# Performance work log

Hardware: AMD Instinct MI355X
Metric: run time of the kernel (lower is better)

Reference implementation:

```python
import jax, jax.numpy as jnp
import numpy as np

N_E = 4096
E_DIM = 512
LEGACY = 0.2


def setup_inputs() -> dict:
    key = jax.random.key(0)
    k1, k2 = jax.random.split(key)
    B, T = 32, 512
    key_soft = jax.random.normal(k1, (B, T, E_DIM), dtype=jnp.float32)
    zero_ts_mask = jnp.zeros((B,), dtype=bool)
    # embedding table has 1 + n_e rows, uniform(-1/n_e, 1/n_e)
    emb = jax.random.uniform(k2, (N_E + 1, E_DIM), dtype=jnp.float32,
                             minval=-1.0 / N_E, maxval=1.0 / N_E)
    return {"key_soft": key_soft, "emb": emb, "zero_ts_mask": zero_ts_mask}


def _neighbor_scan(d, zero_ts_mask):
    # d: [B, T, N+1] squared distances (no grad needed for indices)
    n_e = d.shape[-1] - 1
    ind0 = jnp.clip(jnp.argmin(d[:, 0, :], axis=1), 0, n_e - 1)
    ind0 = jnp.where(zero_ts_mask, 0, ind0)

    def step(ind, d_t):  # ind: [B], d_t: [B, N+1]
        d_here = jnp.take_along_axis(d_t, ind[:, None], axis=1)[:, 0]
        ind_next = jnp.clip(ind + 1, 0, n_e - 1)
        d_next = jnp.take_along_axis(d_t, ind_next[:, None], axis=1)[:, 0]
        ind_new = jnp.where(d_here <= d_next, ind, ind_next)
        return ind_new, ind_new

    d_rest = jnp.transpose(d[:, 1:, :], (1, 0, 2))  # [T-1, B, N+1]
    _, inds_rest = jax.lax.scan(step, ind0, d_rest)
    # [B, T]
    return jnp.concatenate([ind0[:, None], inds_rest.T], axis=1)


def reference(key_soft, emb, zero_ts_mask):
    B, T, D = key_soft.shape
    n_e = emb.shape[0] - 1
    ks_flat = key_soft.reshape(-1, D)
    # squared euclidean distance to every codebook row: [B*T, n_e+1]
    d = (jnp.sum(ks_flat ** 2, axis=1, keepdims=True)
         + jnp.sum(emb ** 2, axis=1)
         - 2.0 * jnp.einsum('bd,nd->bn', ks_flat, emb))
    d_ng = jax.lax.stop_gradient(d)
    min_indices = jnp.argmin(d_ng, axis=1)  # [B*T]
    encoding_indices = _neighbor_scan(d_ng.reshape(B, T, n_e + 1), zero_ts_mask)
    ind_flat = encoding_indices.reshape(-1)

    key_hard_here = emb[ind_flat].reshape(B, T, D)
    key_hard_next = emb[jnp.clip(ind_flat + 1, 0, n_e - 1)].reshape(B, T, D)
    key_min = emb[min_indices].reshape(B, T, D)

    sg = jax.lax.stop_gradient
    ks_sg = sg(key_soft)
    loss_here_base = (jnp.sum((ks_sg - key_hard_here) ** 2, axis=-1) * LEGACY
                      + jnp.sum((key_soft - sg(key_hard_here)) ** 2, axis=-1))
    loss_next_base = (jnp.sum((ks_sg - key_hard_next) ** 2, axis=-1) * LEGACY
                      + jnp.sum((key_soft - sg(key_hard_next)) ** 2, axis=-1))
    loss_min_indices = (jnp.sum((ks_sg - key_min) ** 2, axis=-1)
                        + jnp.sum((key_soft - sg(key_min)) ** 2, axis=-1) * LEGACY)
    loss_here = loss_here_base - jnp.where(loss_min_indices < loss_here_base,
                                           loss_min_indices, 0.0)
    loss_next = loss_next_base - jnp.where(loss_min_indices < loss_next_base,
                                           loss_min_indices, 0.0)

    # straight-through estimator
    key_hard = key_soft + sg(key_hard_here - key_soft)

    v = jnp.max(jnp.max(encoding_indices, axis=1) - jnp.min(encoding_indices, axis=1))
    return key_hard, encoding_indices, v, loss_here, loss_next
```

## Files before the change

kernel.cpp:

```cpp
#include <hip/hip_runtime.h>
#include <cstdint>
#include <cstddef>

#define N_E    4096
#define NCOL   4097
#define DEMB   512
#define BROWS  16384
#define TLEN   512
#define BB     32
#define NTM    128
#define NTN    33
#define NWG    (NTM*NTN)

typedef __attribute__((ext_vector_type(8))) short short8;
typedef __attribute__((ext_vector_type(4))) float f4;

#define WS_KSQ   0
#define WS_ESQ   (WS_KSQ + BROWS*4)
#define WS_PMVB  (WS_ESQ + 4160*4)
#define WS_PMIB  (WS_PMVB + NTN*BROWS*4)
#define WS_DFB   (WS_PMIB + NTN*BROWS*4)
#define WS_DLB   (WS_DFB + NTN*BROWS*4)
#define WS_PMVF  (WS_DLB + NTN*BROWS*4)
#define WS_PMIF  (WS_PMVF + BROWS*4)
#define WS_ENC   (WS_PMIF + BROWS*4)
#define WS_VMAX  (WS_ENC + BROWS*4)
#define WS_MOVE  (WS_VMAX + 512)

__device__ __forceinline__ void cvtpair(float x0, float x1, unsigned int& h, unsigned int& l) {
    asm("v_cvt_pk_bf16_f32 %0, %1, %2" : "=v"(h) : "v"(x0), "v"(x1));
    float h0 = __uint_as_float(h << 16);
    float h1 = __uint_as_float(h & 0xFFFF0000u);
    float l0 = x0 - h0, l1 = x1 - h1;
    asm("v_cvt_pk_bf16_f32 %0, %1, %2" : "=v"(l) : "v"(l0), "v"(l1));
}

__global__ __launch_bounds__(256) void k_sq(const float* __restrict__ ks,
                                            const float* __restrict__ emb,
                                            float* __restrict__ ksq,
                                            float* __restrict__ esq) {
    const int w = threadIdx.x >> 6, lane = threadIdx.x & 63;
    const int row = blockIdx.x * 4 + w;
    if (row >= BROWS + NCOL) return;
    const float* src = (row < BROWS) ? (ks + (size_t)row * DEMB)
                                     : (emb + (size_t)(row - BROWS) * DEMB);
    float4 v1 = *(const float4*)(src + lane * 8);
    float4 v2 = *(const float4*)(src + lane * 8 + 4);
    float s = v1.x*v1.x + v1.y*v1.y + v1.z*v1.z + v1.w*v1.w
            + v2.x*v2.x + v2.y*v2.y + v2.z*v2.z + v2.w*v2.w;
    #pragma unroll
    for (int off = 32; off; off >>= 1) s += __shfl_down(s, off, 64);
    if (lane == 0) {
        if (row < BROWS) ksq[row] = s;
        else             esq[row - BROWS] = s;
    }
}

__global__ __launch_bounds__(256, 2) void k_dist(const float* __restrict__ ks,
                                                 const float* __restrict__ emb,
                                                 const float* __restrict__ ksq,
                                                 const float* __restrict__ esq,
                                                 float* __restrict__ pminvB,
                                                 int*   __restrict__ pminiB,
                                                 float* __restrict__ dfB,
                                                 float* __restrict__ dlB,
                                                 unsigned short* __restrict__ mb16) {
    const int t   = threadIdx.x;
    const int bid = blockIdx.x;
    const int swz = (bid & 7) * (NWG / 8) + (bid >> 3);
    const int mt  = swz / NTN, nt = swz % NTN;
    const int row0 = mt * 128, n0 = nt * 128;

    __shared__ short lds[2][4][128 * 40];

    const int sr = t >> 1, sh = t & 1;
    const float* ap = ks + (size_t)(row0 + sr) * DEMB + sh * 16;
    const int bc = min(n0 + sr, NCOL - 1);
    const float* bp = emb + (size_t)bc * DEMB + sh * 16;
    const int wA = sr * 40 + sh * 16;

    const int w = t >> 6, lane = t & 63;
    const int wm = w >> 1, wn = w & 1;
    const int lq = lane >> 4, lr = lane & 15;
    int aoff[4], boff[4];
    #pragma unroll
    for (int i = 0; i < 4; ++i) aoff[i] = (wm*64 + i*16 + lr)*40 + lq*8;
    #pragma unroll
    for (int j = 0; j < 4; ++j) boff[j] = (wn*64 + j*16 + lr)*40 + lq*8;

    f4 acc[4][4];
    const f4 fz = {0.f, 0.f, 0.f, 0.f};
    #pragma unroll
    for (int i = 0; i < 4; ++i)
        #pragma unroll
        for (int j = 0; j < 4; ++j) acc[i][j] = fz;

    float4 la0, la1, la2, la3, lb0, lb1, lb2, lb3;

    auto do_loads = [&](int s) {
        const float* p = ap + s * 32;
        la0 = *(const float4*)p;       la1 = *(const float4*)(p + 4);
        la2 = *(const float4*)(p + 8); la3 = *(const float4*)(p + 12);
        const float* q = bp + s * 32;
        lb0 = *(const float4*)q;       lb1 = *(const float4*)(q + 4);
        lb2 = *(const float4*)(q + 8); lb3 = *(const float4*)(q + 12);
    };
    auto do_cw = [&](int cb) {
        unsigned int h0,h1,h2,h3,h4,h5,h6,h7, g0,g1,g2,g3,g4,g5,g6,g7;
        cvtpair(la0.x, la0.y, h0, g0); cvtpair(la0.z, la0.w, h1, g1);
        cvtpair(la1.x, la1.y, h2, g2); cvtpair(la1.z, la1.w, h3, g3);
        cvtpair(la2.x, la2.y, h4, g4); cvtpair(la2.z, la2.w, h5, g5);
        cvtpair(la3.x, la3.y, h6, g6); cvtpair(la3.z, la3.w, h7, g7);
        *(uint4*)(&lds[cb][0][wA])     = (uint4){h0,h1,h2,h3};
        *(uint4*)(&lds[cb][0][wA + 8]) = (uint4){h4,h5,h6,h7};
        *(uint4*)(&lds[cb][1][wA])     = (uint4){g0,g1,g2,g3};
        *(uint4*)(&lds[cb][1][wA + 8]) = (uint4){g4,g5,g6,g7};
        cvtpair(lb0.x, lb0.y, h0, g0); cvtpair(lb0.z, lb0.w, h1, g1);
        cvtpair(lb1.x, lb1.y, h2, g2); cvtpair(lb1.z, lb1.w, h3, g3);
        cvtpair(lb2.x, lb2.y, h4, g4); cvtpair(lb2.z, lb2.w, h5, g5);
        cvtpair(lb3.x, lb3.y, h6, g6); cvtpair(lb3.z, lb3.w, h7, g7);
        *(uint4*)(&lds[cb][2][wA])     = (uint4){h0,h1,h2,h3};
        *(uint4*)(&lds[cb][2][wA + 8]) = (uint4){h4,h5,h6,h7};
        *(uint4*)(&lds[cb][3][wA])     = (uint4){g0,g1,g2,g3};
        *(uint4*)(&lds[cb][3][wA + 8]) = (uint4){g4,g5,g6,g7};
    };
    auto do_mm = [&](int cb) {
        short8 fAh[4], fAl[4], fBh[4], fBl[4];
        #pragma unroll
        for (int i = 0; i < 4; ++i) {
            fAh[i] = *(const short8*)(&lds[cb][0][aoff[i]]);
            fAl[i] = *(const short8*)(&lds[cb][1][aoff[i]]);
        }
        #pragma unroll
        for (int j = 0; j < 4; ++j) {
            fBh[j] = *(const short8*)(&lds[cb][2][boff[j]]);
            fBl[j] = *(const short8*)(&lds[cb][3][boff[j]]);
        }
        #pragma unroll
        for (int i = 0; i < 4; ++i)
            #pragma unroll
            for (int j = 0; j < 4; ++j)
                acc[i][j] = __builtin_amdgcn_mfma_f32_16x16x32_bf16(fAh[i], fBh[j], acc[i][j], 0, 0, 0);
        #pragma unroll
        for (int i = 0; i < 4; ++i)
            #pragma unroll
            for (int j = 0; j < 4; ++j)
                acc[i][j] = __builtin_amdgcn_mfma_f32_16x16x32_bf16(fAh[i], fBl[j], acc[i][j], 0, 0, 0);
        #pragma unroll
        for (int i = 0; i < 4; ++i)
            #pragma unroll
            for (int j = 0; j < 4; ++j)
                acc[i][j] = __builtin_amdgcn_mfma_f32_16x16x32_bf16(fAl[i], fBh[j], acc[i][j], 0, 0, 0);
    };

    do_loads(0); do_cw(0); __syncthreads();
    for (int s2 = 0; s2 < 7; ++s2) {
        do_loads(2*s2 + 1); do_mm(0); do_cw(1); __syncthreads();
        do_loads(2*s2 + 2); do_mm(1); do_cw(0); __syncthreads();
    }
    do_loads(15); do_mm(0); do_cw(1); __syncthreads();
    do_mm(1);
    __syncthreads();

    float* sv0 = (float*)&lds[0][0][0];
    int*   si0 = (int*)(sv0 + 256);
    float* sdl = (float*)(si0 + 256);
    float* sdf = sdl + 128;
    float* sd0 = sdf + 128;
    float* sd1 = sd0 + 128;

    const int colC = n0 + wn * 64;
    float esqv[4];
    #pragma unroll
    for (int j = 0; j < 4; ++j) esqv[j] = esq[min(colC + j*16 + lr, NCOL - 1)];

    #pragma unroll
    for (int i = 0; i < 4; ++i) {
        #pragma unroll
        for (int r2 = 0; r2 < 4; ++r2) {
            const int rowl = wm*64 + i*16 + lq*4 + r2;
            const int R = row0 + rowl;
            const float kq = ksq[R];
            float dj[4];
            #pragma unroll
            for (int j = 0; j < 4; ++j) {
                float dd = fmaf(-2.f, acc[i][j][r2], kq + esqv[j]);
                dj[j] = (colC + j*16 + lr <= NCOL - 1) ? dd : 3.0e38f;
            }
            float bv = dj[0]; int bi = colC + lr;
            #pragma unroll
            for (int j = 1; j < 4; ++j) {
                int c = colC + j*16 + lr;
                if (dj[j] < bv || (dj[j] == bv && c < bi)) { bv = dj[j]; bi = c; }
            }
            #pragma unroll
            for (int off = 1; off < 16; off <<= 1) {
                float ov = __shfl_xor(bv, off, 64); int oi = __shfl_xor(bi, off, 64);
                if (ov < bv || (ov == bv && oi < bi)) { bv = ov; bi = oi; }
            }
            if (lr == 0) {
                sv0[rowl*2 + wn] = bv; si0[rowl*2 + wn] = bi;
                if (wn == 1) sdf[rowl] = dj[0];
                else         sd0[rowl] = dj[0];
            }
            if (lr == 15) {
                if (wn == 0) sdl[rowl] = dj[3];
                else         sd1[rowl] = dj[3];
            }
            #pragma unroll
            for (int j = 0; j < 4; ++j) {
                float left = __shfl_up(dj[j], 1, 64);
                if (j > 0) {
                    float ph = __shfl(dj[j-1], (lane & 48) | 15, 64);
                    if (lr == 0) left = ph;
                }
                bool pred = (lr == 0 && j == 0) ? false : (left > dj[j]);
                unsigned long long bal = __ballot(pred);
                const int Cb = colC + j * 16;
                if (lr == 0 && Cb < 4096)
                    mb16[(size_t)R*256 + (Cb >> 4)] = (unsigned short)((bal >> (lq*16)) & 0xFFFFull);
            }
        }
    }
    __syncthreads();
    if (t < 128) {
        const int R = row0 + t;
        float v0 = sv0[t*2], v1 = sv0[t*2+1];
        int   i0 = si0[t*2], i1 = si0[t*2+1];
        const bool sel = (v1 < v0 || (v1 == v0 && i1 < i0));
        pminvB[nt*BROWS + R] = sel ? v1 : v0;
        pminiB[nt*BROWS + R] = sel ? i1 : i0;
        dfB[nt*BROWS + R] = sd0[t];
        dlB[nt*BROWS + R] = sd1[t];
        if (nt < 32 && sdl[t] > sdf[t]) {
            uint8_t* mbyte = (uint8_t*)mb16 + (size_t)R*512 + 16*nt + 8;
            *mbyte = (uint8_t)(*mbyte | 1u);
        }
    }
}

__global__ __launch_bounds__(256) void k_bnd(const float* __restrict__ pminvB,
                                             const int*   __restrict__ pminiB,
                                             const float* __restrict__ dfB,
                                             const float* __restrict__ dlB,
                                             float* __restrict__ pminvF,
                                             int*   __restrict__ pminiF,
                                             uint8_t* __restrict__ movebits) {
    const int w = threadIdx.x >> 6, lane = threadIdx.x & 63;
    const int m = blockIdx.x * 4 + w;
    float bv = 3.0e38f; int bi = 0x7fffffff;
    if (lane < NTN) { bv = pminvB[lane*BROWS + m]; bi = pminiB[lane*BROWS + m]; }
    #pragma unroll
    for (int off = 1; off < 64; off <<= 1) {
        float ov = __shfl_xor(bv, off, 64); int oi = __shfl_xor(bi, off, 64);
        if (ov < bv || (ov == bv && oi < bi)) { bv = ov; bi = oi; }
    }
    if (lane == 0) { pminvF[m] = bv; pminiF[m] = bi; }
    if (lane >= 1 && lane < 32) {
        bool b = dlB[(lane-1)*BROWS + m] > dfB[lane*BROWS + m];
        if (b) {
            uint8_t* p = movebits + (size_t)m * 512 + 16 * lane;
            *p = (uint8_t)(*p | 1u);
        }
    }
}

__global__ __launch_bounds__(64) void k_scan(const int* __restrict__ pminiF,
                                             const uint8_t* __restrict__ mask,
                                             const uint8_t* __restrict__ movebits,
                                             int* __restrict__ enc,
                                             int* __restrict__ vmax) {
    const int b = blockIdx.x;
    const int lane = threadIdx.x;
    const int row0 = b * TLEN;

    int j = min(pminiF[row0], N_E - 1);
    if (mask[b]) j = 0;
    const int jstart = j;

    for (int c = 0; c < 8; ++c) {
        const int t = c * 64 + lane;
        const uint32_t* rowp = (const uint32_t*)(movebits + (size_t)(row0 + t) * 512);
        const int D0a = min((j >> 5) & ~3, 120);
        uint4 wlo = *(const uint4*)(rowp + D0a);
        uint4 whi = *(const uint4*)(rowp + D0a + 4);
        int myenc = j;
        for (int tt = 0; tt < 64; ++tt) {
            const int tglob = c * 64 + tt;
            if (tglob > 0) {
                int q  = j + 1;
                int wi = (q >> 5) - D0a;
                uint32_t sel = wi == 0 ? wlo.x : wi == 1 ? wlo.y : wi == 2 ? wlo.z :
                               wi == 3 ? wlo.w : wi == 4 ? whi.x : wi == 5 ? whi.y :
                               wi == 6 ? whi.z : whi.w;
                uint32_t word = __shfl(sel, tt, 64);
                int bit = (word >> (q & 31)) & 1;
                if (j < N_E - 1) j += bit;
            }
            if (lane == tt) myenc = j;
        }
        enc[row0 + c * 64 + lane] = myenc;
    }
    if (lane == 0) atomicMax(vmax, j - jstart);
}

__global__ __launch_bounds__(256) void k_loss(const float* __restrict__ ks,
                                              const float* __restrict__ emb,
                                              const int*   __restrict__ pminiF,
                                              const int*   __restrict__ enc,
                                              const int*   __restrict__ vmax,
                                              float* __restrict__ out) {
    const int w = threadIdx.x >> 6, lane = threadIdx.x & 63;
    const int row = blockIdx.x * 4 + w;

    float* key_hard = out;
    float* encf     = out + (size_t)BROWS * DEMB;
    float* vout     = encf + BROWS;
    float* lh       = vout + 1;
    float* ln       = lh + BROWS;

    if (blockIdx.x == 0 && threadIdx.x == 0) vout[0] = (float)(*vmax);

    const int j  = enc[row];
    const int jn = min(j + 1, N_E - 1);
    const int mi = pminiF[row];

    const float* ksp = ks  + (size_t)row * DEMB + lane * 8;
    const float* eh  = emb + (size_t)j   * DEMB + lane * 8;
    const float* en  = emb + (size_t)jn  * DEMB + lane * 8;
    const float* em  = emb + (size_t)mi  * DEMB + lane * 8;

    float4 ka = *(const float4*)ksp,     kb = *(const float4*)(ksp + 4);
    float4 ha = *(const float4*)eh,      hb = *(const float4*)(eh + 4);
    float4 na = *(const float4*)en,      nb = *(const float4*)(en + 4);
    float4 ma = *(const float4*)em,      mb = *(const float4*)(em + 4);

    float sh = 0.f, sn = 0.f, sm = 0.f;
    {
        float t;
        t = ka.x-ha.x; sh += t*t;  t = ka.y-ha.y; sh += t*t;
        t = ka.z-ha.z; sh += t*t;  t = ka.w-ha.w; sh += t*t;
        t = kb.x-hb.x; sh += t*t;  t = kb.y-hb.y; sh += t*t;
        t = kb.z-hb.z; sh += t*t;  t = kb.w-hb.w; sh += t*t;
        t = ka.x-na.x; sn += t*t;  t = ka.y-na.y; sn += t*t;
        t = ka.z-na.z; sn += t*t;  t = ka.w-na.w; sn += t*t;
        t = kb.x-nb.x; sn += t*t;  t = kb.y-nb.y; sn += t*t;
        t = kb.z-nb.z; sn += t*t;  t = kb.w-nb.w; sn += t*t;
        t = ka.x-ma.x; sm += t*t;  t = ka.y-ma.y; sm += t*t;
        t = ka.z-ma.z; sm += t*t;  t = ka.w-ma.w; sm += t*t;
        t = kb.x-mb.x; sm += t*t;  t = kb.y-mb.y; sm += t*t;
        t = kb.z-mb.z; sm += t*t;  t = kb.w-mb.w; sm += t*t;
    }
    #pragma unroll
    for (int off = 32; off; off >>= 1) {
        sh += __shfl_down(sh, off, 64);
        sn += __shfl_down(sn, off, 64);
        sm += __shfl_down(sm, off, 64);
    }

    *(float4*)(key_hard + (size_t)row * DEMB + lane * 8)     = ha;
    *(float4*)(key_hard + (size_t)row * DEMB + lane * 8 + 4) = hb;

    if (lane == 0) {
        float bh = sh * 0.2f + sh;
        float bn = sn * 0.2f + sn;
        float lm = sm + sm * 0.2f;
        lh[row]   = bh - (lm < bh ? lm : 0.f);
        ln[row]   = bn - (lm < bn ? lm : 0.f);
        encf[row] = (float)j;
    }
}

extern "C" void kernel_launch(void* const* d_in, const int* in_sizes, int n_in,
                              void* d_out, int out_size, void* d_ws, size_t ws_size,
                              hipStream_t stream) {
    const float*   ks   = (const float*)d_in[0];
    const float*   emb  = (const float*)d_in[1];
    const uint8_t* mask = (const uint8_t*)d_in[2];
    float* out = (float*)d_out;
    uint8_t* ws = (uint8_t*)d_ws;

    float* ksq    = (float*)(ws + WS_KSQ);
    float* esq    = (float*)(ws + WS_ESQ);
    float* pminvB = (float*)(ws + WS_PMVB);
    int*   pminiB = (int*)(ws + WS_PMIB);
    float* dfB    = (float*)(ws + WS_DFB);
    float* dlB    = (float*)(ws + WS_DLB);
    float* pminvF = (float*)(ws + WS_PMVF);
    int*   pminiF = (int*)(ws + WS_PMIF);
    int*   enc    = (int*)(ws + WS_ENC);
    int*   vmax   = (int*)(ws + WS_VMAX);
    uint8_t* movebits = ws + WS_MOVE;

    hipMemsetAsync(vmax, 0, 4, stream);
    k_sq  <<<(BROWS + NCOL + 3) / 4, 256, 0, stream>>>(ks, emb, ksq, esq);
    k_dist<<<NWG, 256, 0, stream>>>(ks, emb, ksq, esq, pminvB, pminiB,
                                    dfB, dlB, (unsigned short*)movebits);
    k_bnd <<<BROWS / 4, 256, 0, stream>>>(pminvB, pminiB, dfB, dlB, pminvF, pminiF, movebits);
    k_scan<<<BB, 64, 0, stream>>>(pminiF, mask, movebits, enc, vmax);
    k_loss<<<BROWS / 4, 256, 0, stream>>>(ks, emb, pminiF, enc, vmax, out);
}
```

Before: 619.4 us.

## Single-buffer MFMA fragment-ordered LDS layout and raise k_dist occupancy to 4 waves

The distance GEMM kernel now stages each k-slice into a single LDS buffer (32 KB instead of 80 KB double-buffered padded rows). The data is laid out in MFMA fragment order, so each lane reads its short8 operands contiguously. Launch bounds rise from 2 to 4 blocks per CU to hide latency through occupancy rather than in-block double buffering. The cost is an extra barrier per k-step and tighter register limits under the new launch bound, which may cause spills given the 64-float accumulator tile.

```diff
diff --git a/kernel.cpp b/kernel.cpp
--- a/kernel.cpp
+++ b/kernel.cpp
@@ -56,7 +56,7 @@
     }
 }
 
-__global__ __launch_bounds__(256, 2) void k_dist(const float* __restrict__ ks,
+__global__ __launch_bounds__(256, 4) void k_dist(const float* __restrict__ ks,
                                                  const float* __restrict__ emb,
                                                  const float* __restrict__ ksq,
                                                  const float* __restrict__ esq,
@@ -71,22 +71,19 @@
     const int mt  = swz / NTN, nt = swz % NTN;
     const int row0 = mt * 128, n0 = nt * 128;
 
-    __shared__ short lds[2][4][128 * 40];
-
-    const int sr = t >> 1, sh = t & 1;
-    const float* ap = ks + (size_t)(row0 + sr) * DEMB + sh * 16;
-    const int bc = min(n0 + sr, NCOL - 1);
-    const float* bp = emb + (size_t)bc * DEMB + sh * 16;
-    const int wA = sr * 40 + sh * 16;
+    __shared__ short lds4[4][4096];
+
+    const int r0 = ((t >> 6) << 4) + (t & 15);
+    const int kq = ((t >> 4) & 3) * 8;
+    const float* apA  = ks  + (size_t)(row0 + r0)      * DEMB + kq;
+    const float* apA2 = ks  + (size_t)(row0 + r0 + 64) * DEMB + kq;
+    const float* apB  = emb + (size_t)min(n0 + r0,      NCOL - 1) * DEMB + kq;
+    const float* apB2 = emb + (size_t)min(n0 + r0 + 64, NCOL - 1) * DEMB + kq;
+    const int w0 = t * 8, w1 = (t + 256) * 8;
 
     const int w = t >> 6, lane = t & 63;
     const int wm = w >> 1, wn = w & 1;
     const int lq = lane >> 4, lr = lane & 15;
-    int aoff[4], boff[4];
-    #pragma unroll
-    for (int i = 0; i < 4; ++i) aoff[i] = (wm*64 + i*16 + lr)*40 + lq*8;
-    #pragma unroll
-    for (int j = 0; j < 4; ++j) boff[j] = (wn*64 + j*16 + lr)*40 + lq*8;
 
     f4 acc[4][4];
     const f4 fz = {0.f, 0.f, 0.f, 0.f};
@@ -98,43 +95,44 @@
     float4 la0, la1, la2, la3, lb0, lb1, lb2, lb3;
 
     auto do_loads = [&](int s) {
-        const float* p = ap + s * 32;
-        la0 = *(const float4*)p;       la1 = *(const float4*)(p + 4);
-        la2 = *(const float4*)(p + 8); la3 = *(const float4*)(p + 12);
-        const float* q = bp + s * 32;
-        lb0 = *(const float4*)q;       lb1 = *(const float4*)(q + 4);
-        lb2 = *(const float4*)(q + 8); lb3 = *(const float4*)(q + 12);
+        const float* p;
+        p = apA  + s * 32; la0 = *(const float4*)p; la1 = *(const float4*)(p + 4);
+        p = apA2 + s * 32; la2 = *(const float4*)p; la3 = *(const float4*)(p + 4);
+        p = apB  + s * 32; lb0 = *(const float4*)p; lb1 = *(const float4*)(p + 4);
+        p = apB2 + s * 32; lb2 = *(const float4*)p; lb3 = *(const float4*)(p + 4);
     };
-    auto do_cw = [&](int cb) {
-        unsigned int h0,h1,h2,h3,h4,h5,h6,h7, g0,g1,g2,g3,g4,g5,g6,g7;
-        cvtpair(la0.x, la0.y, h0, g0); cvtpair(la0.z, la0.w, h1, g1);
-        cvtpair(la1.x, la1.y, h2, g2); cvtpair(la1.z, la1.w, h3, g3);
-        cvtpair(la2.x, la2.y, h4, g4); cvtpair(la2.z, la2.w, h5, g5);
-        cvtpair(la3.x, la3.y, h6, g6); cvtpair(la3.z, la3.w, h7, g7);
-        *(uint4*)(&lds[cb][0][wA])     = (uint4){h0,h1,h2,h3};
-        *(uint4*)(&lds[cb][0][wA + 8]) = (uint4){h4,h5,h6,h7};
-        *(uint4*)(&lds[cb][1][wA])     = (uint4){g0,g1,g2,g3};
-        *(uint4*)(&lds[cb][1][wA + 8]) = (uint4){g4,g5,g6,g7};
-        cvtpair(lb0.x, lb0.y, h0, g0); cvtpair(lb0.z, lb0.w, h1, g1);
-        cvtpair(lb1.x, lb1.y, h2, g2); cvtpair(lb1.z, lb1.w, h3, g3);
-        cvtpair(lb2.x, lb2.y, h4, g4); cvtpair(lb2.z, lb2.w, h5, g5);
-        cvtpair(lb3.x, lb3.y, h6, g6); cvtpair(lb3.z, lb3.w, h7, g7);
-        *(uint4*)(&lds[cb][2][wA])     = (uint4){h0,h1,h2,h3};
-        *(uint4*)(&lds[cb][2][wA + 8]) = (uint4){h4,h5,h6,h7};
-        *(uint4*)(&lds[cb][3][wA])     = (uint4){g0,g1,g2,g3};
-        *(uint4*)(&lds[cb][3][wA + 8]) = (uint4){g4,g5,g6,g7};
+    auto do_cw = [&]() {
+        unsigned int h0,h1,h2,h3, g0,g1,g2,g3;
+        cvtpair(la0.x,la0.y,h0,g0); cvtpair(la0.z,la0.w,h1,g1);
+        cvtpair(la1.x,la1.y,h2,g2); cvtpair(la1.z,la1.w,h3,g3);
+        *(uint4*)&lds4[0][w0] = (uint4){h0,h1,h2,h3};
+        *(uint4*)&lds4[1][w0] = (uint4){g0,g1,g2,g3};
+        cvtpair(la2.x,la2.y,h0,g0); cvtpair(la2.z,la2.w,h1,g1);
+        cvtpair(la3.x,la3.y,h2,g2); cvtpair(la3.z,la3.w,h3,g3);
+        *(uint4*)&lds4[0][w1] = (uint4){h0,h1,h2,h3};
+        *(uint4*)&lds4[1][w1] = (uint4){g0,g1,g2,g3};
+        cvtpair(lb0.x,lb0.y,h0,g0); cvtpair(lb0.z,lb0.w,h1,g1);
+        cvtpair(lb1.x,lb1.y,h2,g2); cvtpair(lb1.z,lb1.w,h3,g3);
+        *(uint4*)&lds4[2][w0] = (uint4){h0,h1,h2,h3};
+        *(uint4*)&lds4[3][w0] = (uint4){g0,g1,g2,g3};
+        cvtpair(lb2.x,lb2.y,h0,g0); cvtpair(lb2.z,lb2.w,h1,g1);
+        cvtpair(lb3.x,lb3.y,h2,g2); cvtpair(lb3.z,lb3.w,h3,g3);
+        *(uint4*)&lds4[2][w1] = (uint4){h0,h1,h2,h3};
+        *(uint4*)&lds4[3][w1] = (uint4){g0,g1,g2,g3};
     };
-    auto do_mm = [&](int cb) {
+    auto do_mm = [&]() {
         short8 fAh[4], fAl[4], fBh[4], fBl[4];
         #pragma unroll
         for (int i = 0; i < 4; ++i) {
-            fAh[i] = *(const short8*)(&lds[cb][0][aoff[i]]);
-            fAl[i] = *(const short8*)(&lds[cb][1][aoff[i]]);
+            const int off = ((wm * 4 + i) * 64 + lane) * 8;
+            fAh[i] = *(const short8*)&lds4[0][off];
+            fAl[i] = *(const short8*)&lds4[1][off];
         }
         #pragma unroll
         for (int j = 0; j < 4; ++j) {
-            fBh[j] = *(const short8*)(&lds[cb][2][boff[j]]);
-            fBl[j] = *(const short8*)(&lds[cb][3][boff[j]]);
+            const int off = ((wn * 4 + j) * 64 + lane) * 8;
+            fBh[j] = *(const short8*)&lds4[2][off];
+            fBl[j] = *(const short8*)&lds4[3][off];
         }
         #pragma unroll
         for (int i = 0; i < 4; ++i)
@@ -153,16 +151,17 @@
                 acc[i][j] = __builtin_amdgcn_mfma_f32_16x16x32_bf16(fAl[i], fBh[j], acc[i][j], 0, 0, 0);
     };
 
-    do_loads(0); do_cw(0); __syncthreads();
-    for (int s2 = 0; s2 < 7; ++s2) {
-        do_loads(2*s2 + 1); do_mm(0); do_cw(1); __syncthreads();
-        do_loads(2*s2 + 2); do_mm(1); do_cw(0); __syncthreads();
-    }
-    do_loads(15); do_mm(0); do_cw(1); __syncthreads();
-    do_mm(1);
+    do_loads(0);
+    for (int s = 0; s < 16; ++s) {
+        __syncthreads();
+        do_cw();
+        __syncthreads();
+        if (s < 15) do_loads(s + 1);
+        do_mm();
+    }
     __syncthreads();
 
-    float* sv0 = (float*)&lds[0][0][0];
+    float* sv0 = (float*)&lds4[0][0];
     int*   si0 = (int*)(sv0 + 256);
     float* sdl = (float*)(si0 + 256);
     float* sdf = sdl + 128;
@@ -180,11 +179,11 @@
         for (int r2 = 0; r2 < 4; ++r2) {
             const int rowl = wm*64 + i*16 + lq*4 + r2;
             const int R = row0 + rowl;
-            const float kq = ksq[R];
+            const float kq2 = ksq[R];
             float dj[4];
             #pragma unroll
             for (int j = 0; j < 4; ++j) {
-                float dd = fmaf(-2.f, acc[i][j][r2], kq + esqv[j]);
+                float dd = fmaf(-2.f, acc[i][j][r2], kq2 + esqv[j]);
                 dj[j] = (colC + j*16 + lr <= NCOL - 1) ? dd : 3.0e38f;
             }
             float bv = dj[0]; int bi = colC + lr;
```

Measured after the change: 949.0 us. +53.2%, slower.
